# Kernel tuning notes

Hardware: AMD Instinct MI355X
Metric: run time of the kernel (lower is better)

## Reference

```python
import jax, jax.numpy as jnp
import numpy as np

DIM = 1024
TOPK = 64
PAIRS = DIM // 2  # phase_pairs default
PHASE_MIX = 0.5
GATE_THRESHOLD = 0.0
EPS = 1e-12  # F.normalize default eps


def _l2norm(v):
    # matches F.normalize(v, dim=-1): v / max(||v||, eps)
    n = jnp.linalg.norm(v, axis=-1, keepdims=True)
    return v / jnp.maximum(n, EPS)


def setup_inputs() -> dict:
    key = jax.random.key(0)
    ks = jax.random.split(key, 6)
    s = 0.02  # small init scale for weights
    return {
        "x": jax.random.normal(ks[0], (4, 4096, DIM), dtype=jnp.float32),
        "gate_W": jax.random.normal(ks[1], (DIM, DIM), dtype=jnp.float32) * s,
        "gate_b": jnp.zeros((DIM,), dtype=jnp.float32),
        "mag_W": jax.random.normal(ks[2], (DIM, DIM), dtype=jnp.float32) * s,
        "mag_b": jnp.zeros((DIM,), dtype=jnp.float32),
        "Wq": jax.random.normal(ks[3], (DIM, DIM), dtype=jnp.float32) * s,
        "Wk": jax.random.normal(ks[4], (DIM, DIM), dtype=jnp.float32) * s,
        "phase_W": jax.random.normal(ks[5], (2 * PAIRS, DIM), dtype=jnp.float32) * s,
    }


def reference(x, gate_W, gate_b, mag_W, mag_b, Wq, Wk, phase_W):
    B, S, D = x.shape
    # gated SAE-style projection (gated=True, diag=False)
    gate_pre = x @ gate_W.T + gate_b          # [B,S,D]
    mag_pre = x @ mag_W.T + mag_b             # [B,S,D]
    # hard gate with straight-through estimator
    gate_soft = jax.nn.sigmoid(gate_pre)
    gate_hard = (gate_pre > GATE_THRESHOLD).astype(x.dtype)
    gate = gate_hard + gate_soft - jax.lax.stop_gradient(gate_soft)
    mag = jax.nn.relu(mag_pre)
    # top-k scatter mask along feature dim
    idx = jax.lax.top_k(gate_pre, TOPK)[1]    # [B,S,K]
    rows = jnp.arange(B * S)[:, None]
    mask = (jnp.zeros((B * S, D), dtype=bool)
            .at[rows, idx.reshape(B * S, TOPK)].set(True)
            .reshape(B, S, D))
    gate = jnp.where(mask, gate, jnp.zeros_like(gate))
    mag = jnp.where(mask, mag, jnp.zeros_like(mag))
    xg = gate * mag
    # twist projections, L2-normalized
    q = _l2norm(xg @ Wq.T)
    k = _l2norm(xg @ Wk.T)
    # symplectic momentum map over consecutive steps
    momentum_map = q[:, 1:] * k[:, :-1] - q[:, :-1] * k[:, 1:]  # [B,S-1,D]
    twist_mag = jnp.linalg.norm(momentum_map, axis=-1, keepdims=True)
    complexity = jnp.pad(jnp.tanh(twist_mag), ((0, 0), (1, 0), (0, 0)))  # [B,S,1]
    # phase branch (phase_mix > 0)
    phase = (xg @ phase_W.T).reshape(B, S, PAIRS, 2)
    phase = _l2norm(phase)
    pp, pc = phase[:, :-1], phase[:, 1:]
    cross = pp[..., 0] * pc[..., 1] - pp[..., 1] * pc[..., 0]   # [B,S-1,P]
    dot = jnp.clip(jnp.sum(pp * pc, axis=-1), -1.0, 1.0)
    phase_delta = jnp.abs(jnp.arctan2(cross, dot)) / jnp.pi
    phase_score = jnp.pad(jnp.mean(phase_delta, axis=-1, keepdims=True),
                          ((0, 0), (1, 0), (0, 0)))             # [B,S,1]
    return (1.0 - PHASE_MIX) * complexity + PHASE_MIX * phase_score
```

## Files before the change

kernel.cpp:

```cpp
#include <hip/hip_runtime.h>
#include <math.h>

#define DIM 1024
#define ROWS 16384
#define SEQ 4096
#define MARGIN 0.012f
#define MAXC 24

typedef __bf16 v8bf __attribute__((ext_vector_type(8)));
typedef float v4f __attribute__((ext_vector_type(4)));
typedef int v8i __attribute__((ext_vector_type(8)));

__device__ __forceinline__ unsigned short f2bf(float f){
  unsigned u = __float_as_uint(f);
  u = u + 0x7FFFu + ((u >> 16) & 1u);
  return (unsigned short)(u >> 16);
}
__device__ __forceinline__ float bf2f(unsigned short h){
  return __uint_as_float(((unsigned)h) << 16);
}
__device__ __forceinline__ unsigned short relu_bf(unsigned short h){
  return (h & 0x8000u) ? (unsigned short)0 : h;
}
__device__ __forceinline__ unsigned f2fp8(float f){
  float a = fabsf(f);
  unsigned sign = (__float_as_uint(f) >> 24) & 0x80u;
  if (a >= 448.f) return sign | 0x7Eu;
  if (a < 0.015625f){
    int k = (int)rintf(a * 512.f);
    if (k >= 8) return sign | 0x08u;
    return sign | (unsigned)k;
  }
  unsigned u = __float_as_uint(a);
  u += 0x7FFFFu + ((u >> 20) & 1u);
  int e = (int)((u >> 23) & 0xFFu) - 127;
  unsigned m = (u >> 20) & 7u;
  if (e > 8) return sign | 0x7Eu;
  return sign | ((unsigned)(e + 7) << 3) | m;
}
__device__ __forceinline__ void lds_fence(){
  __asm__ volatile("s_waitcnt lgkmcnt(0)" ::: "memory");
}

__global__ __launch_bounds__(256) void cvt_all(
    const float* __restrict__ x,
    const float* __restrict__ w0, const float* __restrict__ w1,
    const float* __restrict__ w2, const float* __restrict__ w3,
    const float* __restrict__ w4,
    unsigned short* __restrict__ xbf, unsigned short* __restrict__ wbf,
    unsigned char* __restrict__ wf8){
  const int y = blockIdx.y;
  int i = (blockIdx.x * 256 + threadIdx.x) * 4;
  if (y < 16){
    const float* s = x + ((size_t)y << 20);
    float4 f = *(const float4*)(s + i);
    ushort4 o; o.x = f2bf(f.x); o.y = f2bf(f.y); o.z = f2bf(f.z); o.w = f2bf(f.w);
    *(ushort4*)(xbf + ((size_t)y << 20) + i) = o;
  } else if (y < 18){
    const float* s = (y == 16) ? w0 : w1;
    float4 f = *(const float4*)(s + i);
    ushort4 o; o.x = f2bf(f.x); o.y = f2bf(f.y); o.z = f2bf(f.z); o.w = f2bf(f.w);
    *(ushort4*)(wbf + ((size_t)(y - 16) << 20) + i) = o;
  } else {
    const float* s = (y == 18) ? w2 : ((y == 19) ? w3 : w4);
    float4 f = *(const float4*)(s + i);
    unsigned u = f2fp8(f.x * 32.f) | (f2fp8(f.y * 32.f) << 8) |
                 (f2fp8(f.z * 32.f) << 16) | (f2fp8(f.w * 32.f) << 24);
    *(unsigned*)(wf8 + ((size_t)(y - 18) << 20) + i) = u;
  }
}

#define GBAR() asm volatile("s_barrier" ::: "memory")
#define GLGKM0() { asm volatile("s_waitcnt lgkmcnt(0)" ::: "memory"); __builtin_amdgcn_sched_barrier(0); }
#define GVM4() asm volatile("s_waitcnt vmcnt(4)" ::: "memory")

__global__ __launch_bounds__(512, 2) void gemm_bt(
    const unsigned short* __restrict__ A, const unsigned short* __restrict__ B,
    const float* __restrict__ bias0, const float* __restrict__ bias1,
    unsigned short* __restrict__ C0, unsigned short* __restrict__ C1)
{
  extern __shared__ unsigned char lds[];
  const int t = threadIdx.x;
  const int lane = t & 63, wave = t >> 6;
  const int wr = wave >> 2, wc = wave & 3;
  const int bid = blockIdx.x;
  const int swz = (bid & 7) * 64 + (bid >> 3);
  const int m0 = (swz & 63) * 256;
  const int n0 = (swz >> 6) * 256;

  int offv[4];
#pragma unroll
  for (int h = 0; h < 2; h++)
#pragma unroll
    for (int i = 0; i < 2; i++){
      int o = h * 16384 + i * 8192 + t * 16;
      int u = o ^ (((o >> 9) & 1) << 5);
      int r = ((u >> 11) << 4) | ((u >> 6) & 15);
      int c = (((u >> 10) & 1) << 5) | ((u & 63) >> 1);
      offv[h * 2 + i] = r * 1024 + c;
    }
  const int off00 = offv[0], off01 = offv[1], off10 = offv[2], off11 = offv[3];
  const unsigned short* Ab = A + ((size_t)m0 << 10);
  const unsigned short* Bb = B + ((size_t)n0 << 10);

  const int laneterm = (lane & 15) * 64 + (((lane >> 4) * 16) ^ (((lane >> 3) & 1) * 32));
  const int aBase = wr * 16384 + laneterm;
  const int bBase = 32768 + wc * 8192 + laneterm;

#define GLD1(srcp, dsto) __builtin_amdgcn_global_load_lds( \
    (const __attribute__((address_space(1))) void*)(srcp), \
    (__attribute__((address_space(3))) void*)(lds + (dsto)), 16, 0, 0)

  auto stageA = [&](int h, int kt, int pp){
    const int o0 = h ? off10 : off00, o1 = h ? off11 : off01;
    GLD1(Ab + o0 + kt * 64, pp * 65536 + h * 16384 + t * 16);
    GLD1(Ab + o1 + kt * 64, pp * 65536 + h * 16384 + 8192 + t * 16);
  };
  auto stageB = [&](int h, int kt, int pp){
    const int o0 = h ? off10 : off00, o1 = h ? off11 : off01;
    GLD1(Bb + o0 + kt * 64, pp * 65536 + 32768 + h * 16384 + t * 16);
    GLD1(Bb + o1 + kt * 64, pp * 65536 + 32768 + h * 16384 + 8192 + t * 16);
  };

  v4f acc[8][4];
#pragma unroll
  for (int i = 0; i < 8; i++)
#pragma unroll
    for (int j = 0; j < 4; j++) acc[i][j] = v4f{0.f, 0.f, 0.f, 0.f};

  stageB(0, 0, 0); stageB(1, 0, 0);
  stageA(0, 0, 0); stageA(1, 0, 0);
  stageB(0, 1, 1); stageB(1, 1, 1);
  GVM4();
  GBAR();

  int p = 0;
  for (int X = 0; X < 16; X++, p ^= 1){
    const int pb = p * 65536;
    const int ktA = (X + 1 < 16) ? X + 1 : 15;
    const int ktB = (X + 2 < 16) ? X + 2 : X;
    v8bf a0[8], a1[8], b0[4], b1[4];

#pragma unroll
    for (int mi = 0; mi < 8; mi++) a0[mi] = *(const v8bf*)(lds + pb + aBase + mi * 2048);
#pragma unroll
    for (int ni = 0; ni < 4; ni++) b0[ni] = *(const v8bf*)(lds + pb + bBase + ni * 2048);
    stageA(0, ktA, p ^ 1);
    GBAR();
    __builtin_amdgcn_s_setprio(1);
#pragma unroll
    for (int mi = 0; mi < 4; mi++)
#pragma unroll
      for (int ni = 0; ni < 4; ni++)
        acc[mi][ni] = __builtin_amdgcn_mfma_f32_16x16x32_bf16(a0[mi], b0[ni], acc[mi][ni], 0, 0, 0);
    __builtin_amdgcn_s_setprio(0);
    GBAR();

#pragma unroll
    for (int mi = 0; mi < 4; mi++) a1[mi] = *(const v8bf*)(lds + pb + aBase + 1024 + mi * 2048);
#pragma unroll
    for (int ni = 0; ni < 4; ni++) b1[ni] = *(const v8bf*)(lds + pb + bBase + 1024 + ni * 2048);
    stageA(1, ktA, p ^ 1);
    GBAR();
    __builtin_amdgcn_s_setprio(1);
#pragma unroll
    for (int mi = 0; mi < 4; mi++)
#pragma unroll
      for (int ni = 0; ni < 4; ni++)
        acc[4 + mi][ni] = __builtin_amdgcn_mfma_f32_16x16x32_bf16(a0[4 + mi], b0[ni], acc[4 + mi][ni], 0, 0, 0);
    __builtin_amdgcn_s_setprio(0);
    GLGKM0();
    GBAR();

#pragma unroll
    for (int mi = 4; mi < 8; mi++) a1[mi] = *(const v8bf*)(lds + pb + aBase + 1024 + mi * 2048);
    stageB(0, ktB, p);
    GBAR();
    __builtin_amdgcn_s_setprio(1);
#pragma unroll
    for (int mi = 0; mi < 4; mi++)
#pragma unroll
      for (int ni = 0; ni < 4; ni++)
        acc[mi][ni] = __builtin_amdgcn_mfma_f32_16x16x32_bf16(a1[mi], b1[ni], acc[mi][ni], 0, 0, 0);
    __builtin_amdgcn_s_setprio(0);
    GBAR();

    stageB(1, ktB, p);
    GBAR();
    __builtin_amdgcn_s_setprio(1);
#pragma unroll
    for (int mi = 0; mi < 4; mi++)
#pragma unroll
      for (int ni = 0; ni < 4; ni++)
        acc[4 + mi][ni] = __builtin_amdgcn_mfma_f32_16x16x32_bf16(a1[4 + mi], b1[ni], acc[4 + mi][ni], 0, 0, 0);
    __builtin_amdgcn_s_setprio(0);
    GVM4();
    GBAR();
  }

  const int os = n0 >> 10;
  unsigned short* Cp = (os == 0) ? C0 : C1;
  const float* bp = (os == 0) ? bias0 : bias1;
  const int ar = lane & 15, aq = lane >> 4;
  const int ncol0 = (n0 & (DIM - 1)) + wc * 64;
#pragma unroll
  for (int ni = 0; ni < 4; ni++){
    const int col = ncol0 + ni * 16 + ar;
    const float bv = bp[col];
#pragma unroll
    for (int mi = 0; mi < 8; mi++){
#pragma unroll
      for (int rr = 0; rr < 4; rr++){
        int rowg = m0 + wr * 128 + mi * 16 + aq * 4 + rr;
        Cp[(size_t)rowg * DIM + col] = f2bf(acc[mi][ni][rr] + bv);
      }
    }
  }
  asm volatile("s_waitcnt vmcnt(0)" ::: "memory");
}

__global__ __launch_bounds__(256, 3) void gemm8(
    const unsigned char* __restrict__ A, const unsigned char* __restrict__ B,
    unsigned short* __restrict__ C0, unsigned short* __restrict__ C1,
    unsigned short* __restrict__ C2)
{
  __shared__ unsigned char lA[128 * 128];
  __shared__ unsigned char lB[128 * 128];
  const int t = threadIdx.x;
  const int lane = t & 63, wave = t >> 6;
  const int bid = blockIdx.y * gridDim.x + blockIdx.x;
  const int m0 = (bid & 127) * 128;
  const int n0 = (bid >> 7) * 128;
  const int wm = (wave >> 1) * 64, wn = (wave & 1) * 64;
  const int ar = lane & 15, aq = lane >> 4;

  v4f acc[4][4];
#pragma unroll
  for (int i = 0; i < 4; i++)
#pragma unroll
    for (int j = 0; j < 4; j++) acc[i][j] = v4f{0.f, 0.f, 0.f, 0.f};

  for (int k0 = 0; k0 < DIM; k0 += 128){
#pragma unroll
    for (int i = 0; i < 4; i++){
      int c = (wave * 4 + i) * 64 + lane;
      int row = c >> 3, kq = c & 7;
      __builtin_amdgcn_global_load_lds(
        (const __attribute__((address_space(1))) void*)(A + (size_t)(m0 + row) * DIM + k0 + kq * 16),
        (__attribute__((address_space(3))) void*)(&lA[c * 16]), 16, 0, 0);
      __builtin_amdgcn_global_load_lds(
        (const __attribute__((address_space(1))) void*)(B + (size_t)(n0 + row) * DIM + k0 + kq * 16),
        (__attribute__((address_space(3))) void*)(&lB[c * 16]), 16, 0, 0);
    }
    __syncthreads();
    v8i a8[4], b8[4];
#pragma unroll
    for (int i = 0; i < 4; i++){
      a8[i] = *(const v8i*)&lA[(wm + i * 16 + ar) * 128 + aq * 32];
      b8[i] = *(const v8i*)&lB[(wn + i * 16 + ar) * 128 + aq * 32];
    }
#pragma unroll
    for (int mi = 0; mi < 4; mi++)
#pragma unroll
      for (int ni = 0; ni < 4; ni++)
        acc[mi][ni] = __builtin_amdgcn_mfma_scale_f32_16x16x128_f8f6f4(
            a8[mi], b8[ni], acc[mi][ni], 0, 0, 0, 127u, 0, 127u);
    __syncthreads();
  }

  const int os = n0 >> 10;
  unsigned short* Cp = (os == 0) ? C0 : ((os == 1) ? C1 : C2);
#pragma unroll
  for (int mi = 0; mi < 4; mi++)
#pragma unroll
    for (int ni = 0; ni < 4; ni++){
      int col = (n0 + wn + ni * 16 + ar) & (DIM - 1);
#pragma unroll
      for (int rr = 0; rr < 4; rr++){
        int rowg = m0 + wm + mi * 16 + aq * 4 + rr;
        Cp[(size_t)rowg * DIM + col] = f2bf(acc[mi][ni][rr] * 0.03125f);
      }
    }
}

__global__ __launch_bounds__(256) void select_k(
  const unsigned short* __restrict__ gate_pre, const unsigned short* __restrict__ mag_pre,
  const float* __restrict__ x, const float* __restrict__ gW, const float* __restrict__ gb,
  unsigned char* __restrict__ xg8)
{
  __shared__ int   s_cnt[4];
  __shared__ int   s_idx[4][MAXC];
  __shared__ float s_ex [4][MAXC];
  __shared__ int   s_res[4][MAXC];

  const int t = threadIdx.x;
  const int lane = t & 63, wave = t >> 6;
  const int r = blockIdx.x * 4 + wave;
  const size_t rb = (size_t)r * DIM;

  float vg[16], vx[16];
  unsigned short mg[16];
#pragma unroll
  for (int c = 0; c < 4; c++){
    ushort4 g4 = *(const ushort4*)(gate_pre + rb + c * 256 + lane * 4);
    float4 x4 = *(const float4*)(x          + rb + c * 256 + lane * 4);
    ushort4 m4 = *(const ushort4*)(mag_pre  + rb + c * 256 + lane * 4);
    vg[c*4+0]=bf2f(g4.x); vg[c*4+1]=bf2f(g4.y); vg[c*4+2]=bf2f(g4.z); vg[c*4+3]=bf2f(g4.w);
    vx[c*4+0]=x4.x; vx[c*4+1]=x4.y; vx[c*4+2]=x4.z; vx[c*4+3]=x4.w;
    mg[c*4+0]=m4.x; mg[c*4+1]=m4.y; mg[c*4+2]=m4.z; mg[c*4+3]=m4.w;
  }
  if (lane == 0) s_cnt[wave] = 0;

  float lo = -8.f, hi = 8.f;
#pragma unroll
  for (int it = 0; it < 15; it++){
    float mid = 0.5f * (lo + hi);
    int cn = 0;
#pragma unroll
    for (int e = 0; e < 16; e++) cn += (vg[e] > mid) ? 1 : 0;
#pragma unroll
    for (int m = 32; m; m >>= 1) cn += __shfl_xor(cn, m);
    if (cn >= 64) lo = mid; else hi = mid;
  }
  const float cl = lo - MARGIN, ch = hi + MARGIN;

  int n1 = 0;
#pragma unroll
  for (int e = 0; e < 16; e++) n1 += (vg[e] > ch) ? 1 : 0;
#pragma unroll
  for (int m = 32; m; m >>= 1) n1 += __shfl_xor(n1, m);
  const int s = 64 - n1;

  lds_fence();
#pragma unroll
  for (int e = 0; e < 16; e++){
    float vv = vg[e];
    if (vv >= cl && vv <= ch){
      int p = atomicAdd(&s_cnt[wave], 1);
      if (p < MAXC) s_idx[wave][p] = (e >> 2) * 256 + lane * 4 + (e & 3);
    }
  }
  lds_fence();
  int namb = s_cnt[wave]; if (namb > MAXC) namb = MAXC;

  for (int i = 0; i < namb; i++){
    int d = s_idx[wave][i];
    const float* wr = gW + (size_t)d * DIM;
    float p = 0.f;
#pragma unroll
    for (int c = 0; c < 4; c++){
      float4 w4 = *(const float4*)(wr + c * 256 + lane * 4);
      p = fmaf(vx[c*4+0], w4.x, p); p = fmaf(vx[c*4+1], w4.y, p);
      p = fmaf(vx[c*4+2], w4.z, p); p = fmaf(vx[c*4+3], w4.w, p);
    }
#pragma unroll
    for (int m = 32; m; m >>= 1) p += __shfl_xor(p, m);
    if (lane == 0) s_ex[wave][i] = p + gb[d];
  }
  lds_fence();

  if (lane < namb){
    float e = s_ex[wave][lane]; int d = s_idx[wave][lane];
    int rank = 0;
    for (int j = 0; j < namb; j++){
      float ej = s_ex[wave][j]; int dj = s_idx[wave][j];
      if (ej > e || (ej == e && dj < d)) rank++;
    }
    s_res[wave][lane] = (rank < s && e > 0.f) ? 1 : 0;
  }
  lds_fence();

  float vals[16];
#pragma unroll
  for (int e = 0; e < 16; e++)
    vals[e] = (vg[e] > ch && vg[e] > 0.f) ? bf2f(relu_bf(mg[e])) : 0.f;
  for (int i = 0; i < namb; i++){
    int d = s_idx[wave][i];
    int res = s_res[wave][i];
    if (((d >> 2) & 63) == lane){
      int e = (d >> 8) * 4 + (d & 3);
      vals[e] = res ? bf2f(relu_bf(mg[e])) : 0.f;
    }
  }
#pragma unroll
  for (int c = 0; c < 4; c++){
    unsigned u = f2fp8(vals[c*4+0]) | (f2fp8(vals[c*4+1]) << 8) |
                 (f2fp8(vals[c*4+2]) << 16) | (f2fp8(vals[c*4+3]) << 24);
    *(unsigned*)(xg8 + rb + c * 256 + lane * 4) = u;
  }
}

__global__ __launch_bounds__(256) void epilogue_k(
  const unsigned short* __restrict__ q_pre, const unsigned short* __restrict__ k_pre,
  const unsigned short* __restrict__ p_pre, float* __restrict__ out)
{
  const int r0 = blockIdx.x * 4;
  const int t = threadIdx.x;
  const int lane = t & 63, wave = t >> 6;
  __shared__ float red[16];

  const int rp = (r0 == 0) ? 0 : r0 - 1;
  float vqp[4], vkp[4], vpp[4];
  {
    ushort4 uq = *(const ushort4*)(q_pre + (size_t)rp * DIM + 4*t);
    ushort4 uk = *(const ushort4*)(k_pre + (size_t)rp * DIM + 4*t);
    ushort4 up = *(const ushort4*)(p_pre + (size_t)rp * DIM + 4*t);
    vqp[0]=bf2f(uq.x); vqp[1]=bf2f(uq.y); vqp[2]=bf2f(uq.z); vqp[3]=bf2f(uq.w);
    vkp[0]=bf2f(uk.x); vkp[1]=bf2f(uk.y); vkp[2]=bf2f(uk.z); vkp[3]=bf2f(uk.w);
    vpp[0]=bf2f(up.x); vpp[1]=bf2f(up.y); vpp[2]=bf2f(up.z); vpp[3]=bf2f(up.w);
  }
  float aq = 0.f, ak = 0.f;
#pragma unroll
  for (int j = 0; j < 4; j++){ aq = fmaf(vqp[j], vqp[j], aq); ak = fmaf(vkp[j], vkp[j], ak); }
#pragma unroll
  for (int m = 32; m; m >>= 1){ aq += __shfl_xor(aq, m); ak += __shfl_xor(ak, m); }
  if (lane == 0){ red[wave] = aq; red[4 + wave] = ak; }
  __syncthreads();
  float rqp = 1.f / fmaxf(sqrtf(red[0] + red[1] + red[2] + red[3]), 1e-12f);
  float rkp = 1.f / fmaxf(sqrtf(red[4] + red[5] + red[6] + red[7]), 1e-12f);
  __syncthreads();

  for (int rr = 0; rr < 4; rr++){
    const int r = r0 + rr;
    float vqc[4], vkc[4], vpc[4];
    {
      ushort4 uq = *(const ushort4*)(q_pre + (size_t)r * DIM + 4*t);
      ushort4 uk = *(const ushort4*)(k_pre + (size_t)r * DIM + 4*t);
      ushort4 up = *(const ushort4*)(p_pre + (size_t)r * DIM + 4*t);
      vqc[0]=bf2f(uq.x); vqc[1]=bf2f(uq.y); vqc[2]=bf2f(uq.z); vqc[3]=bf2f(uq.w);
      vkc[0]=bf2f(uk.x); vkc[1]=bf2f(uk.y); vkc[2]=bf2f(uk.z); vkc[3]=bf2f(uk.w);
      vpc[0]=bf2f(up.x); vpc[1]=bf2f(up.y); vpc[2]=bf2f(up.z); vpc[3]=bf2f(up.w);
    }
    const bool seg = (r & (SEQ - 1)) == 0;
    float aqc = 0.f, akc = 0.f;
#pragma unroll
    for (int j = 0; j < 4; j++){ aqc = fmaf(vqc[j], vqc[j], aqc); akc = fmaf(vkc[j], vkc[j], akc); }
    float dsum = 0.f;
    if (!seg){
#pragma unroll
      for (int j = 0; j < 2; j++){
        float ax = vpp[2*j], ay = vpp[2*j+1], bx = vpc[2*j], by = vpc[2*j+1];
        float ia = 1.f / fmaxf(sqrtf(ax * ax + ay * ay), 1e-12f);
        float ib = 1.f / fmaxf(sqrtf(bx * bx + by * by), 1e-12f);
        ax *= ia; ay *= ia; bx *= ib; by *= ib;
        float cross = ax * by - ay * bx;
        float dot = fminf(fmaxf(ax * bx + ay * by, -1.f), 1.f);
        dsum += fabsf(atan2f(cross, dot)) * 0.3183098861837907f;
      }
    }
#pragma unroll
    for (int m = 32; m; m >>= 1){
      aqc += __shfl_xor(aqc, m); akc += __shfl_xor(akc, m); dsum += __shfl_xor(dsum, m);
    }
    if (lane == 0){ red[wave] = aqc; red[4 + wave] = akc; red[8 + wave] = dsum; }
    __syncthreads();
    float rqc = 1.f / fmaxf(sqrtf(red[0] + red[1] + red[2] + red[3]), 1e-12f);
    float rkc = 1.f / fmaxf(sqrtf(red[4] + red[5] + red[6] + red[7]), 1e-12f);
    if (!seg){
      float tw = 0.f;
#pragma unroll
      for (int j = 0; j < 4; j++){
        float m = (vqc[j] * rqc) * (vkp[j] * rkp) - (vqp[j] * rqp) * (vkc[j] * rkc);
        tw = fmaf(m, m, tw);
      }
#pragma unroll
      for (int m = 32; m; m >>= 1) tw += __shfl_xor(tw, m);
      if (lane == 0) red[12 + wave] = tw;
      __syncthreads();
      if (t == 0){
        float dtot = red[8] + red[9] + red[10] + red[11];
        float twt = red[12] + red[13] + red[14] + red[15];
        out[r] = 0.5f * tanhf(sqrtf(twt)) + 0.5f * (dtot * (1.f / 512.f));
      }
    } else {
      if (t == 0) out[r] = 0.f;
    }
    __syncthreads();
#pragma unroll
    for (int j = 0; j < 4; j++){ vqp[j] = vqc[j]; vkp[j] = vkc[j]; vpp[j] = vpc[j]; }
    rqp = rqc; rkp = rkc;
  }
}

extern "C" void kernel_launch(void* const* d_in, const int* in_sizes, int n_in,
                              void* d_out, int out_size, void* d_ws, size_t ws_size,
                              hipStream_t stream)
{
  const float* x       = (const float*)d_in[0];
  const float* gate_W  = (const float*)d_in[1];
  const float* gate_b  = (const float*)d_in[2];
  const float* mag_W   = (const float*)d_in[3];
  const float* mag_b   = (const float*)d_in[4];
  const float* Wq      = (const float*)d_in[5];
  const float* Wk      = (const float*)d_in[6];
  const float* phase_W = (const float*)d_in[7];
  float* out = (float*)d_out;

  char* ws = (char*)d_ws;
  unsigned short* xbf = (unsigned short*)ws;
  unsigned short* wbf = (unsigned short*)(ws + 33554432);
  unsigned char*  wf8 = (unsigned char*)(ws + 37748736);
  unsigned short* gate_pre = (unsigned short*)(ws + 41943040);
  unsigned short* mag_pre  = (unsigned short*)(ws + 75497472);
  unsigned short* p_pre    = (unsigned short*)(ws + 109051904);
  unsigned short* q_pre = gate_pre;
  unsigned short* k_pre = mag_pre;

  static bool attr_set = false;
  if (!attr_set){
    hipFuncSetAttribute((const void*)gemm_bt,
                        hipFuncAttributeMaxDynamicSharedMemorySize, 131072);
    attr_set = true;
  }

  dim3 b256(256);
  cvt_all<<<dim3(1024, 21), b256, 0, stream>>>(x, gate_W, mag_W, Wq, Wk, phase_W,
                                               xbf, wbf, wf8);

  gemm_bt<<<dim3(512), dim3(512), 131072, stream>>>(xbf, wbf, gate_b, mag_b,
                                                    gate_pre, mag_pre);

  unsigned char* xg8 = (unsigned char*)xbf;
  select_k<<<ROWS / 4, b256, 0, stream>>>(gate_pre, mag_pre, x, gate_W, gate_b, xg8);

  gemm8<<<dim3(24, 128), b256, 0, stream>>>(xg8, wf8, q_pre, k_pre, p_pre);

  epilogue_k<<<ROWS / 4, b256, 0, stream>>>(q_pre, k_pre, p_pre, out);
}
```

Baseline: 385.3 us.

## Stage GEMM epilogues through LDS for coalesced stores and swizzle gemm8 block order

Both GEMM epilogues now write bf16 results into shared memory and then emit 16-byte coalesced row stores, replacing scattered 2-byte column-strided global writes. The fp8 GEMM also remaps block indices so consecutive blocks spread across N tiles, aiming at better L2 reuse of the A rows. The cost is extra LDS traffic and barriers per 16-row chunk of the epilogue.

New measurement: 395.4 us. 2.6% more time.

```diff
diff --git a/kernel.cpp b/kernel.cpp
--- a/kernel.cpp
+++ b/kernel.cpp
@@ -198,23 +198,37 @@
     GBAR();
   }
 
+  asm volatile("s_waitcnt vmcnt(0)" ::: "memory");
+  __syncthreads();
+
   const int os = n0 >> 10;
   unsigned short* Cp = (os == 0) ? C0 : C1;
   const float* bp = (os == 0) ? bias0 : bias1;
+  const int colbase = n0 & (DIM - 1);
+  unsigned short* lt = (unsigned short*)lds;
   const int ar = lane & 15, aq = lane >> 4;
-  const int ncol0 = (n0 & (DIM - 1)) + wc * 64;
-#pragma unroll
-  for (int ni = 0; ni < 4; ni++){
-    const int col = ncol0 + ni * 16 + ar;
-    const float bv = bp[col];
-#pragma unroll
-    for (int mi = 0; mi < 8; mi++){
-#pragma unroll
-      for (int rr = 0; rr < 4; rr++){
-        int rowg = m0 + wr * 128 + mi * 16 + aq * 4 + rr;
-        Cp[(size_t)rowg * DIM + col] = f2bf(acc[mi][ni][rr] + bv);
-      }
-    }
+  const int lrw = wr * 16 + aq * 4;
+  const int lrow = t >> 4;
+  const int cseg = (t & 15) * 16;
+  const size_t grb = (size_t)(m0 + (lrow >> 4) * 128 + (lrow & 15)) * DIM + colbase + cseg;
+  float bv[4];
+#pragma unroll
+  for (int ni = 0; ni < 4; ni++) bv[ni] = bp[colbase + wc * 64 + ni * 16 + ar];
+#pragma unroll
+  for (int mi = 0; mi < 8; mi++){
+#pragma unroll
+    for (int ni = 0; ni < 4; ni++){
+      const int colc = wc * 64 + ni * 16 + ar;
+#pragma unroll
+      for (int rr = 0; rr < 4; rr++)
+        lt[(lrw + rr) * 264 + colc] = f2bf(acc[mi][ni][rr] + bv[ni]);
+    }
+    __syncthreads();
+    uint4 v0 = *(const uint4*)&lt[lrow * 264 + cseg];
+    uint4 v1 = *(const uint4*)&lt[lrow * 264 + cseg + 8];
+    *(uint4*)(Cp + grb + (size_t)mi * 16 * DIM) = v0;
+    *(uint4*)(Cp + grb + (size_t)mi * 16 * DIM + 8) = v1;
+    __syncthreads();
   }
   asm volatile("s_waitcnt vmcnt(0)" ::: "memory");
 }
@@ -228,9 +242,10 @@
   __shared__ unsigned char lB[128 * 128];
   const int t = threadIdx.x;
   const int lane = t & 63, wave = t >> 6;
-  const int bid = blockIdx.y * gridDim.x + blockIdx.x;
-  const int m0 = (bid & 127) * 128;
-  const int n0 = (bid >> 7) * 128;
+  const int bid0 = blockIdx.y * gridDim.x + blockIdx.x;
+  const int swz = (bid0 & 7) * 384 + (bid0 >> 3);
+  const int m0 = (swz & 127) * 128;
+  const int n0 = (swz >> 7) * 128;
   const int wm = (wave >> 1) * 64, wn = (wave & 1) * 64;
   const int ar = lane & 15, aq = lane >> 4;
 
@@ -270,17 +285,29 @@
 
   const int os = n0 >> 10;
   unsigned short* Cp = (os == 0) ? C0 : ((os == 1) ? C1 : C2);
-#pragma unroll
-  for (int mi = 0; mi < 4; mi++)
+  const int colbase = n0 & (DIM - 1);
+  unsigned short* lt = (unsigned short*)lA;
+  const int lrw = (wave >> 1) * 16 + aq * 4;
+  const int colc0 = (wave & 1) * 64;
+  const int lrow = t >> 3;
+  const int cseg = (t & 7) * 16;
+  const size_t grb = (size_t)(m0 + (lrow >> 4) * 64 + (lrow & 15)) * DIM + colbase + cseg;
+#pragma unroll
+  for (int mi = 0; mi < 4; mi++){
 #pragma unroll
     for (int ni = 0; ni < 4; ni++){
-      int col = (n0 + wn + ni * 16 + ar) & (DIM - 1);
-#pragma unroll
-      for (int rr = 0; rr < 4; rr++){
-        int rowg = m0 + wm + mi * 16 + aq * 4 + rr;
-        Cp[(size_t)rowg * DIM + col] = f2bf(acc[mi][ni][rr] * 0.03125f);
-      }
-    }
+      const int colc = colc0 + ni * 16 + ar;
+#pragma unroll
+      for (int rr = 0; rr < 4; rr++)
+        lt[(lrw + rr) * 136 + colc] = f2bf(acc[mi][ni][rr] * 0.03125f);
+    }
+    __syncthreads();
+    uint4 v0 = *(const uint4*)&lt[lrow * 136 + cseg];
+    uint4 v1 = *(const uint4*)&lt[lrow * 136 + cseg + 8];
+    *(uint4*)(Cp + grb + (size_t)mi * 16 * DIM) = v0;
+    *(uint4*)(Cp + grb + (size_t)mi * 16 * DIM + 8) = v1;
+    __syncthreads();
+  }
 }
 
 __global__ __launch_bounds__(256) void select_k(
```
